# Kernel tuning notes

Measured on AMD Instinct MI355X. Metric: run time of the kernel, lower is better.

## Reference

```python
import jax, jax.numpy as jnp
import numpy as np

N_WAY = 5
K_SHOT = 5
TEMPERATURE = 0.2
EPS = 1e-12  # torch F.normalize eps


def setup_inputs() -> dict:
    key = jax.random.key(0)
    k1, k2, k3, k4 = jax.random.split(key, 4)
    b, q, c, h, w = 4, 75, 640, 10, 10
    s = N_WAY * K_SHOT
    return {
        "support_xf": jax.random.normal(k1, (b, s, c, h, w), dtype=jnp.float32),
        "support_y": jax.random.randint(k2, (b, s), 0, N_WAY),
        "query_xf": jax.random.normal(k3, (b, q, c, h, w), dtype=jnp.float32),
        "query_y": jax.random.randint(k4, (b, q), 0, N_WAY),
    }


def _l2norm(x):
    # normalize along last axis (channel), matching F.normalize semantics
    n = jnp.sqrt(jnp.sum(x * x, axis=-1, keepdims=True))
    return x / jnp.maximum(n, EPS)


def _inner_simi(support_xf, query_xf):
    # cosine similarity between all query local descriptors and all support
    # local descriptors, grouped per class -> [b, q, N, M_q, M_s]
    b, s, c, h, w = support_xf.shape
    q = query_xf.shape[1]
    hw = h * w
    Ms = K_SHOT * hw
    sx = support_xf.reshape(b, N_WAY, K_SHOT, c, hw)
    sx = jnp.transpose(sx, (0, 1, 2, 4, 3)).reshape(b, N_WAY, Ms, c)  # [b,N,M_s,c]
    qx = jnp.transpose(query_xf.reshape(b, q, c, hw), (0, 1, 3, 2))  # [b,q,M_q,c]
    return jnp.einsum('bqmc,bnsc->bqnms', _l2norm(qx), _l2norm(sx))


def _dmnn_mask(simi):
    # simi: [b,q,N,M_q,M_s] -> bool mask [b,q,M_q]
    b, q, N, Mq, Ms = simi.shape
    merged = jnp.transpose(simi, (0, 1, 3, 2, 4)).reshape(b, q, Mq, N * Ms)
    query_nearest = jnp.argmax(merged, axis=-1)            # [b,q,M_q] global NN idx
    class_max = jnp.max(simi, axis=-1)                      # [b,q,N,M_q]
    top2 = jax.lax.top_k(jnp.transpose(class_max, (0, 1, 3, 2)), 2)[0]  # [b,q,M_q,2]
    query_class_diff = top2[..., 0] - top2[..., 1]          # [b,q,M_q]
    diffs_m = jax.nn.one_hot(query_nearest, N * Ms, dtype=simi.dtype) \
        * query_class_diff[..., None]                       # [b,q,M_q,N*M_s]
    diffs_max_nearest = jnp.argmax(diffs_m, axis=-2)        # [b,q,N*M_s]
    gathered = jnp.take_along_axis(diffs_max_nearest, query_nearest, axis=-1)  # [b,q,M_q]
    return gathered == jnp.arange(Mq)[None, None, :]


def reference(support_xf, support_y, query_xf, query_y):
    b, q = query_xf.shape[0], query_xf.shape[1]
    simi = _inner_simi(support_xf, query_xf)                # [b,q,N,M_q,M_s]
    q_mask = _dmnn_mask(simi)                               # [b,q,M_q]
    class_max = jnp.max(simi, axis=-1)                      # [b,q,N,M_q]
    query_value = jnp.sum(class_max * q_mask[:, :, None, :].astype(simi.dtype), axis=-1)
    logits = query_value.reshape(b * q, N_WAY) / TEMPERATURE
    logp = jax.nn.log_softmax(logits, axis=-1)
    labels = query_y.reshape(b * q)
    loss = -jnp.mean(jnp.take_along_axis(logp, labels[:, None], axis=1))
    return loss
```

## Files before the change

kernel.cpp:

```cpp
#include <hip/hip_runtime.h>
#include <math.h>

#define B 4
#define Q 75
#define NBQ (B*Q)
#define NWAY 5
#define KSHOT 5
#define C 640
#define HW 100
#define MS 500
#define SLAB (C*HW)

#define MT32_B 236
#define RT_B 472
#define A_CHUNKS_B (RT_B*20*64)
#define S_CHUNKS_ALL (20*32*20*64)
#define S_CHUNKS_B   (5*32*20*64)

#define CHI 0.00390625f
#define CLO 1.9073486328125e-06f

typedef _Float16 half8 __attribute__((ext_vector_type(8)));
typedef float f32x4 __attribute__((ext_vector_type(4)));

__device__ __forceinline__ void gl_lds16(const void* gsrc, void* ldst) {
  __builtin_amdgcn_global_load_lds(
      (const __attribute__((address_space(1))) unsigned int*)gsrc,
      (__attribute__((address_space(3))) unsigned int*)ldst, 16, 0, 0);
}

#define WS_BASE 340352ull
#define NEED_ALL   104908288ull
#define NEED_PERB   46908928ull
#define NEED_PERB2  27248128ull

__global__ __launch_bounds__(256) void norm_kernel(const float* __restrict__ s_xf,
                                                   const float* __restrict__ q_xf,
                                                   float* __restrict__ invs,
                                                   float* __restrict__ invq) {
  int id = blockIdx.x;
  const float* base;
  float* out;
  if (id < 100) { base = s_xf + (size_t)id * SLAB;        out = invs + id * HW; }
  else          { base = q_xf + (size_t)(id - 100) * SLAB; out = invq + (id - 100) * HW; }
  __shared__ float ssum[2][HW];
  int t = threadIdx.x;
  if (t < 2 * HW) ((float*)ssum)[t] = 0.f;
  __syncthreads();
  if (t < 2 * HW) {
    int p = t % HW, half = t / HW;
    float part = 0.f;
    for (int ch = half * 320; ch < half * 320 + 320; ++ch) {
      float v = base[ch * HW + p];
      part = fmaf(v, v, part);
    }
    ssum[half][p] = part;
  }
  __syncthreads();
  if (t < HW) {
    float nrm = sqrtf(ssum[0][t] + ssum[1][t]);
    out[t] = 1.f / fmaxf(nrm, 1e-12f);
  }
}

__device__ __forceinline__ void dual_split(float w, _Float16* h0, _Float16* h1) {
  _Float16 a = (_Float16)w;
  *h0 = a;
  *h1 = (_Float16)((w - (float)a) * 2048.f);
}

__global__ __launch_bounds__(256) void convs_kernel(const float* __restrict__ s_xf,
                                                    const float* __restrict__ invs,
                                                    uint4* __restrict__ o0,
                                                    uint4* __restrict__ o1,
                                                    int bn0) {
  int id = blockIdx.x * 256 + threadIdx.x;
  int lane = id & 63;
  int tmp = id >> 6;
  int ks = tmp % 20;
  int t2 = tmp / 20;
  int jf = t2 % 32;
  int bnl = t2 / 32;
  int bn = bn0 + bnl;
  int j = jf * 16 + (lane & 15);
  int k = ks * 32 + (lane >> 4) * 8;
  union { _Float16 h[8]; uint4 u; } p0, p1;
  if (j < MS) {
    int s = j / 100, p = j % 100;
    int slab = bn * 5 + s;
    const float* src = s_xf + ((size_t)slab * 640 + k) * 100 + p;
    float sc = invs[slab * 100 + p] * 16.f;
#pragma unroll
    for (int kj = 0; kj < 8; ++kj)
      dual_split(src[kj * 100] * sc, &p0.h[kj], &p1.h[kj]);
  } else {
    p0.u = make_uint4(0, 0, 0, 0);
    p1.u = make_uint4(0, 0, 0, 0);
  }
  o0[id] = p0.u; o1[id] = p1.u;
}

__global__ __launch_bounds__(256) void convq_kernel(const float* __restrict__ q_xf,
                                                    const float* __restrict__ invq,
                                                    uint4* __restrict__ o0,
                                                    uint4* __restrict__ o1,
                                                    int b0) {
  int id = blockIdx.x * 256 + threadIdx.x;
  int bloc = id / A_CHUNKS_B;
  int c = id % A_CHUNKS_B;
  int bb = b0 + bloc;
  int lane = c & 63;
  int tmp = c >> 6;
  int ks = tmp % 20;
  int rt = tmp / 20;
  int row = rt * 16 + (lane & 15);
  int k = ks * 32 + (lane >> 4) * 8;
  union { _Float16 h[8]; uint4 u; } p0, p1;
  if (row < Q * HW) {
    int qi = row / 100, p = row % 100;
    const float* src = q_xf + ((size_t)(bb * Q + qi) * 640 + k) * 100 + p;
    float sc = invq[(bb * Q + qi) * 100 + p] * 16.f;
#pragma unroll
    for (int kj = 0; kj < 8; ++kj)
      dual_split(src[kj * 100] * sc, &p0.h[kj], &p1.h[kj]);
  } else {
    p0.u = make_uint4(0, 0, 0, 0);
    p1.u = make_uint4(0, 0, 0, 0);
  }
  o0[id] = p0.u; o1[id] = p1.u;
}

__global__ __launch_bounds__(256, 3) void gemm_kernel(
    const uint4* __restrict__ a0, const uint4* __restrict__ a1,
    const uint4* __restrict__ b0p, const uint4* __restrict__ b1p,
    float* __restrict__ cmax, int* __restrict__ carg,
    int bq0, int aStride, int sbnBase, int mode ) {
  int wgid = blockIdx.x;
  int x = wgid & 7, s = wgid >> 3;
  int o;
  if (mode == 0) {
    o = x * 590 + s;
  } else {
    if (x < 4) { if (s >= 148) return; o = x * 148 + s; }
    else       { if (s >= 147) return; o = 592 + (x - 4) * 147 + s; }
  }
  int bnloc = o / MT32_B;
  int mt32 = o % MT32_B;
  int bloc = bnloc / 5;
  int n = bnloc % 5;
  int bb = bq0 + bloc;
  const uint4* A0 = a0 + (size_t)bloc * aStride;
  const uint4* A1 = a1 + (size_t)bloc * aStride;
  int bnl = bb * 5 + n - sbnBase;

  __shared__ __align__(16) _Float16 sA[2][2][2][512];
  __shared__ float sV[4][32];
  __shared__ int   sJ[4][32];

  int t = threadIdx.x;
  int w = t >> 6, lane = t & 63;

  if (lane < 32) { sV[w][lane] = -1e30f; sJ[w][lane] = 0; }

#define STAGE_A1(KS, BUF) do {                                                  \
    int limb_ = w >> 1, rtl_ = w & 1;                                           \
    size_t aIdx = ((size_t)(mt32 * 2 + rtl_) * 20 + (KS)) * 64 + lane;          \
    gl_lds16((limb_ ? A1 : A0) + aIdx, (void*)&sA[(BUF)][limb_][rtl_][0]);      \
  } while (0)

  for (int pass = 0; pass < 2; ++pass) {
    int jf0 = pass * 16 + w * 4;
    size_t bBase = (size_t)(bnl * 32 + jf0) * 1280 + lane;

    f32x4 acc0[2][4], accM[2][4];
#pragma unroll
    for (int mf = 0; mf < 2; ++mf)
#pragma unroll
      for (int f = 0; f < 4; ++f) {
        acc0[mf][f] = (f32x4){0.f, 0.f, 0.f, 0.f};
        accM[mf][f] = (f32x4){0.f, 0.f, 0.f, 0.f};
      }

    STAGE_A1(0, 0);
    for (int ks = 0; ks < 20; ++ks) {
      int cur = ks & 1;
      __syncthreads();

      size_t bo = bBase + (size_t)ks * 64;
      half8 bv0[4], bv1[4];
#pragma unroll
      for (int f = 0; f < 4; ++f) bv0[f] = *(const half8*)&b0p[bo + (size_t)f * 1280];
#pragma unroll
      for (int f = 0; f < 4; ++f) bv1[f] = *(const half8*)&b1p[bo + (size_t)f * 1280];
      __builtin_amdgcn_sched_barrier(0);

      if (ks < 19) STAGE_A1(ks + 1, cur ^ 1);
      __builtin_amdgcn_sched_barrier(0);

#pragma unroll
      for (int mf = 0; mf < 2; ++mf) {
        half8 av0 = *(const half8*)&sA[cur][0][mf][lane * 8];
        half8 av1 = *(const half8*)&sA[cur][1][mf][lane * 8];
#pragma unroll
        for (int f = 0; f < 4; ++f) {
          acc0[mf][f] = __builtin_amdgcn_mfma_f32_16x16x32_f16(av0, bv0[f], acc0[mf][f], 0, 0, 0);
          accM[mf][f] = __builtin_amdgcn_mfma_f32_16x16x32_f16(av0, bv1[f], accM[mf][f], 0, 0, 0);
          accM[mf][f] = __builtin_amdgcn_mfma_f32_16x16x32_f16(av1, bv0[f], accM[mf][f], 0, 0, 0);
        }
      }
    }

#pragma unroll
    for (int mf = 0; mf < 2; ++mf)
#pragma unroll
      for (int f = 0; f < 4; ++f) {
        int j = pass * 256 + w * 64 + f * 16 + (lane & 15);
        bool ok = (j < MS);
#pragma unroll
        for (int rg = 0; rg < 4; ++rg) {
          float v = ok ? (acc0[mf][f][rg] * CHI + accM[mf][f][rg] * CLO) : -1e30f;
          int ji = ok ? j : 0x7fffffff;
#pragma unroll
          for (int mk = 1; mk < 16; mk <<= 1) {
            float ov = __shfl_xor(v, mk);
            int oj = __shfl_xor(ji, mk);
            if (ov > v || (ov == v && oj < ji)) { v = ov; ji = oj; }
          }
          if ((lane & 15) == 0) {
            int row32 = mf * 16 + (lane >> 4) * 4 + rg;
            if (v > sV[w][row32]) { sV[w][row32] = v; sJ[w][row32] = ji; }
          }
        }
      }
  }
#undef STAGE_A1

  __syncthreads();
  if (w == 0 && lane < 32) {
    int row32 = lane;
    float v = sV[0][row32];
    int ji = sJ[0][row32];
#pragma unroll
    for (int q4 = 1; q4 < 4; ++q4) {
      float ov = sV[q4][row32];
      int oj = sJ[q4][row32];
      if (ov > v || (ov == v && oj < ji)) { v = ov; ji = oj; }
    }
    int r = mt32 * 32 + row32;
    if (r < Q * HW) {
      int bq = bb * Q + r / 100, p = r % 100;
      size_t oo = (size_t)(bq * NWAY + n) * HW + p;
      cmax[oo] = v;
      carg[oo] = ji;
    }
  }
}

#define TCF 32
#define TJF 64
__global__ __launch_bounds__(256) void simi_kernel(const float* __restrict__ s_xf,
                                                   const float* __restrict__ q_xf,
                                                   const float* __restrict__ invs,
                                                   const float* __restrict__ invq,
                                                   float* __restrict__ cmax,
                                                   int* __restrict__ carg) {
  int id = blockIdx.x;
  int n = id % NWAY;
  int bq = id / NWAY;
  int b = bq / Q;
  const float* qbase = q_xf + (size_t)bq * SLAB;
  const float* sbase = s_xf + (size_t)(b * 25 + n * KSHOT) * SLAB;
  const float* invqB = invq + bq * HW;
  const float* invsB = invs + (b * 2500 + n * MS);

  __shared__ __align__(16) float As[TCF][112];
  __shared__ __align__(16) float Bs[TCF][TJF];
  __shared__ float sInvQ[HW];
  __shared__ float sInvS[MS];

  int t = threadIdx.x;
  for (int i = t; i < HW; i += 256) sInvQ[i] = invqB[i];
  for (int i = t; i < MS; i += 256) sInvS[i] = invsB[i];

  int tj = t & 15, tm = t >> 4;
  float best[7];
  int bidx[7];
#pragma unroll
  for (int r = 0; r < 7; ++r) { best[r] = -1e30f; bidx[r] = 0; }

  for (int jt0 = 0; jt0 < MS; jt0 += TJF) {
    float acc[7][4];
#pragma unroll
    for (int r = 0; r < 7; ++r)
#pragma unroll
      for (int jj = 0; jj < 4; ++jj) acc[r][jj] = 0.f;
    for (int c0 = 0; c0 < C; c0 += TCF) {
      __syncthreads();
      for (int i = t; i < TCF * HW; i += 256) {
        int p = i % HW;
        As[i / HW][p] = qbase[c0 * HW + i] * sInvQ[p];
      }
      for (int i = t; i < TCF * TJF; i += 256) {
        int cc = i / TJF, jj = i % TJF;
        int j = jt0 + jj;
        float v = 0.f;
        if (j < MS) v = sbase[(j / 100) * SLAB + (c0 + cc) * 100 + (j % 100)] * sInvS[j];
        Bs[cc][jj] = v;
      }
      __syncthreads();
#pragma unroll
      for (int cc = 0; cc < TCF; ++cc) {
        float4 bv = *(const float4*)&Bs[cc][tj * 4];
#pragma unroll
        for (int r = 0; r < 7; ++r) {
          float a = As[cc][tm * 7 + r];
          acc[r][0] = fmaf(a, bv.x, acc[r][0]);
          acc[r][1] = fmaf(a, bv.y, acc[r][1]);
          acc[r][2] = fmaf(a, bv.z, acc[r][2]);
          acc[r][3] = fmaf(a, bv.w, acc[r][3]);
        }
      }
    }
#pragma unroll
    for (int r = 0; r < 7; ++r)
#pragma unroll
      for (int jj = 0; jj < 4; ++jj) {
        int j = jt0 + tj * 4 + jj;
        float v = acc[r][jj];
        if (j < MS && v > best[r]) { best[r] = v; bidx[r] = j; }
      }
  }
#pragma unroll
  for (int r = 0; r < 7; ++r)
#pragma unroll
    for (int mask = 1; mask < 16; mask <<= 1) {
      float ov = __shfl_xor(best[r], mask);
      int oi = __shfl_xor(bidx[r], mask);
      if (ov > best[r] || (ov == best[r] && oi < bidx[r])) { best[r] = ov; bidx[r] = oi; }
    }
  if (tj == 0)
#pragma unroll
    for (int r = 0; r < 7; ++r) {
      int m = tm * 7 + r;
      if (m < HW) {
        cmax[(size_t)(bq * NWAY + n) * HW + m] = best[r];
        carg[(size_t)(bq * NWAY + n) * HW + m] = bidx[r];
      }
    }
}

__global__ __launch_bounds__(128) void mask_loss_kernel(const float* __restrict__ cmax,
                                                        const int* __restrict__ carg,
                                                        const int* __restrict__ query_y,
                                                        float* __restrict__ lossv) {
  int bq = blockIdx.x;
  int t = threadIdx.x;
  __shared__ float sDiff[HW];
  __shared__ int sNear[HW];
  __shared__ float sCm[NWAY][HW];
  __shared__ float red[128];

  if (t < HW) {
    float cm[NWAY];
#pragma unroll
    for (int nn = 0; nn < NWAY; ++nn) {
      cm[nn] = cmax[(size_t)(bq * NWAY + nn) * HW + t];
      sCm[nn][t] = cm[nn];
    }
    float v0 = -1e30f, v1 = -1e30f;
#pragma unroll
    for (int nn = 0; nn < NWAY; ++nn) {
      float v = cm[nn];
      if (v > v0) { v1 = v0; v0 = v; }
      else if (v > v1) { v1 = v; }
    }
    sDiff[t] = v0 - v1;
    float gb = -1e30f;
    int gn = 0;
#pragma unroll
    for (int nn = 0; nn < NWAY; ++nn)
      if (cm[nn] > gb) { gb = cm[nn]; gn = nn; }
    sNear[t] = gn * MS + carg[(size_t)(bq * NWAY + gn) * HW + t];
  }
  __syncthreads();

  bool msk = false;
  if (t < HW) {
    int j = sNear[t];
    int wn = 0;
    float wv = -1.f;
    for (int mp = 0; mp < HW; ++mp) {
      float v = (sNear[mp] == j) ? sDiff[mp] : 0.f;
      if (v > wv) { wv = v; wn = mp; }
    }
    msk = (wn == t);
  }

  float qv[NWAY];
#pragma unroll
  for (int nn = 0; nn < NWAY; ++nn) {
    __syncthreads();
    red[t] = (t < HW && msk) ? sCm[nn][t] : 0.f;
    __syncthreads();
    for (int s = 64; s > 0; s >>= 1) {
      if (t < s) red[t] += red[t + s];
      __syncthreads();
    }
    qv[nn] = red[0];
  }

  if (t == 0) {
    float logits[NWAY], mx = -1e30f;
#pragma unroll
    for (int nn = 0; nn < NWAY; ++nn) {
      logits[nn] = qv[nn] / 0.2f;
      mx = fmaxf(mx, logits[nn]);
    }
    float se = 0.f;
#pragma unroll
    for (int nn = 0; nn < NWAY; ++nn) se += expf(logits[nn] - mx);
    float lse = mx + logf(se);
    int label = query_y[bq];
    lossv[bq] = -(logits[label] - lse);
  }
}

__global__ __launch_bounds__(512) void finalize_kernel(const float* __restrict__ lossv,
                                                       float* __restrict__ out) {
  __shared__ float red[512];
  int t = threadIdx.x;
  red[t] = (t < NBQ) ? lossv[t] : 0.f;
  __syncthreads();
  for (int s = 256; s > 0; s >>= 1) {
    if (t < s) red[t] += red[t + s];
    __syncthreads();
  }
  if (t == 0) out[0] = red[0] / (float)NBQ;
}

extern "C" void kernel_launch(void* const* d_in, const int* in_sizes, int n_in,
                              void* d_out, int out_size, void* d_ws, size_t ws_size,
                              hipStream_t stream) {
  const float* s_xf = (const float*)d_in[0];
  const float* q_xf = (const float*)d_in[2];
  const int* query_y = (const int*)d_in[3];

  float* ws = (float*)d_ws;
  float* invs = ws;
  float* invq = ws + 10000;
  float* cmax = ws + 40000;
  int* carg = (int*)(ws + 190000);
  float* lossv = ws + 340000;

  norm_kernel<<<400, 256, 0, stream>>>(s_xf, q_xf, invs, invq);

  const size_t SP_ALL = 3276800, SP_B = 819200, QS_B = 2416640;

  if (ws_size >= NEED_ALL) {
    uint4* S0 = (uint4*)(ws + WS_BASE);
    uint4* S1 = (uint4*)(ws + WS_BASE + SP_ALL);
    uint4* Q0 = (uint4*)(ws + WS_BASE + 2 * SP_ALL);
    uint4* Q1 = (uint4*)(ws + WS_BASE + 2 * SP_ALL + 4 * QS_B);
    convs_kernel<<<S_CHUNKS_ALL / 256, 256, 0, stream>>>(s_xf, invs, S0, S1, 0);
    convq_kernel<<<4 * A_CHUNKS_B / 256, 256, 0, stream>>>(q_xf, invq, Q0, Q1, 0);
    gemm_kernel<<<4720, 256, 0, stream>>>(Q0, Q1, S0, S1,
                                          cmax, carg, 0, A_CHUNKS_B, 0, 0);
  } else if (ws_size >= NEED_PERB) {
    uint4* S0 = (uint4*)(ws + WS_BASE);
    uint4* S1 = (uint4*)(ws + WS_BASE + SP_ALL);
    uint4* Q0 = (uint4*)(ws + WS_BASE + 2 * SP_ALL);
    uint4* Q1 = (uint4*)(ws + WS_BASE + 2 * SP_ALL + QS_B);
    convs_kernel<<<S_CHUNKS_ALL / 256, 256, 0, stream>>>(s_xf, invs, S0, S1, 0);
    for (int b = 0; b < 4; ++b) {
      convq_kernel<<<A_CHUNKS_B / 256, 256, 0, stream>>>(q_xf, invq, Q0, Q1, b);
      gemm_kernel<<<1184, 256, 0, stream>>>(Q0, Q1, S0, S1,
                                            cmax, carg, b, 0, 0, 1);
    }
  } else if (ws_size >= NEED_PERB2) {
    uint4* S0 = (uint4*)(ws + WS_BASE);
    uint4* S1 = (uint4*)(ws + WS_BASE + SP_B);
    uint4* Q0 = (uint4*)(ws + WS_BASE + 2 * SP_B);
    uint4* Q1 = (uint4*)(ws + WS_BASE + 2 * SP_B + QS_B);
    for (int b = 0; b < 4; ++b) {
      convs_kernel<<<S_CHUNKS_B / 256, 256, 0, stream>>>(s_xf, invs, S0, S1, b * 5);
      convq_kernel<<<A_CHUNKS_B / 256, 256, 0, stream>>>(q_xf, invq, Q0, Q1, b);
      gemm_kernel<<<1184, 256, 0, stream>>>(Q0, Q1, S0, S1,
                                            cmax, carg, b, 0, b * 5, 1);
    }
  } else {
    simi_kernel<<<1500, 256, 0, stream>>>(s_xf, q_xf, invs, invq, cmax, carg);
  }

  mask_loss_kernel<<<NBQ, 128, 0, stream>>>(cmax, carg, query_y, lossv);
  finalize_kernel<<<1, 512, 0, stream>>>(lossv, (float*)d_out);
}
```

Measured before the change: 546.2 us.

## Load A fragments directly from global into registers instead of LDS staging

The GEMM kernel previously staged the A-operand tiles (hi/lo limbs) into a double-buffered LDS array via global_load_lds, with a block-wide barrier every k-step. Now each wave loads its own A fragments straight from global memory into registers and drops the barriers and the shared buffer. This removes the per-k-step synchronisation and the LDS traffic, but each of the four waves now fetches the same A data redundantly, relying on the cache. The loop is also kept rolled, so load latency is no longer explicitly overlapped.

```diff
diff --git a/kernel.cpp b/kernel.cpp
--- a/kernel.cpp
+++ b/kernel.cpp
@@ -22,12 +22,6 @@
 
 typedef _Float16 half8 __attribute__((ext_vector_type(8)));
 typedef float f32x4 __attribute__((ext_vector_type(4)));
-
-__device__ __forceinline__ void gl_lds16(const void* gsrc, void* ldst) {
-  __builtin_amdgcn_global_load_lds(
-      (const __attribute__((address_space(1))) unsigned int*)gsrc,
-      (__attribute__((address_space(3))) unsigned int*)ldst, 16, 0, 0);
-}
 
 #define WS_BASE 340352ull
 #define NEED_ALL   104908288ull
@@ -153,7 +147,6 @@
   const uint4* A1 = a1 + (size_t)bloc * aStride;
   int bnl = bb * 5 + n - sbnBase;
 
-  __shared__ __align__(16) _Float16 sA[2][2][2][512];
   __shared__ float sV[4][32];
   __shared__ int   sJ[4][32];
 
@@ -162,11 +155,7 @@
 
   if (lane < 32) { sV[w][lane] = -1e30f; sJ[w][lane] = 0; }
 
-#define STAGE_A1(KS, BUF) do {                                                  \
-    int limb_ = w >> 1, rtl_ = w & 1;                                           \
-    size_t aIdx = ((size_t)(mt32 * 2 + rtl_) * 20 + (KS)) * 64 + lane;          \
-    gl_lds16((limb_ ? A1 : A0) + aIdx, (void*)&sA[(BUF)][limb_][rtl_][0]);      \
-  } while (0)
+  size_t aBase = ((size_t)(mt32 * 2) * 20) * 64 + lane;
 
   for (int pass = 0; pass < 2; ++pass) {
     int jf0 = pass * 16 + w * 4;
@@ -181,10 +170,14 @@
         accM[mf][f] = (f32x4){0.f, 0.f, 0.f, 0.f};
       }
 
-    STAGE_A1(0, 0);
+#pragma unroll 1
     for (int ks = 0; ks < 20; ++ks) {
-      int cur = ks & 1;
-      __syncthreads();
+      size_t ao = aBase + (size_t)ks * 64;
+      half8 a0v[2], a1v[2];
+      a0v[0] = *(const half8*)&A0[ao];
+      a0v[1] = *(const half8*)&A0[ao + 1280];
+      a1v[0] = *(const half8*)&A1[ao];
+      a1v[1] = *(const half8*)&A1[ao + 1280];
 
       size_t bo = bBase + (size_t)ks * 64;
       half8 bv0[4], bv1[4];
@@ -192,20 +185,14 @@
       for (int f = 0; f < 4; ++f) bv0[f] = *(const half8*)&b0p[bo + (size_t)f * 1280];
 #pragma unroll
       for (int f = 0; f < 4; ++f) bv1[f] = *(const half8*)&b1p[bo + (size_t)f * 1280];
-      __builtin_amdgcn_sched_barrier(0);
-
-      if (ks < 19) STAGE_A1(ks + 1, cur ^ 1);
-      __builtin_amdgcn_sched_barrier(0);
 
 #pragma unroll
       for (int mf = 0; mf < 2; ++mf) {
-        half8 av0 = *(const half8*)&sA[cur][0][mf][lane * 8];
-        half8 av1 = *(const half8*)&sA[cur][1][mf][lane * 8];
 #pragma unroll
         for (int f = 0; f < 4; ++f) {
-          acc0[mf][f] = __builtin_amdgcn_mfma_f32_16x16x32_f16(av0, bv0[f], acc0[mf][f], 0, 0, 0);
-          accM[mf][f] = __builtin_amdgcn_mfma_f32_16x16x32_f16(av0, bv1[f], accM[mf][f], 0, 0, 0);
-          accM[mf][f] = __builtin_amdgcn_mfma_f32_16x16x32_f16(av1, bv0[f], accM[mf][f], 0, 0, 0);
+          acc0[mf][f] = __builtin_amdgcn_mfma_f32_16x16x32_f16(a0v[mf], bv0[f], acc0[mf][f], 0, 0, 0);
+          accM[mf][f] = __builtin_amdgcn_mfma_f32_16x16x32_f16(a0v[mf], bv1[f], accM[mf][f], 0, 0, 0);
+          accM[mf][f] = __builtin_amdgcn_mfma_f32_16x16x32_f16(a1v[mf], bv0[f], accM[mf][f], 0, 0, 0);
         }
       }
     }
@@ -233,7 +220,6 @@
         }
       }
   }
-#undef STAGE_A1
 
   __syncthreads();
   if (w == 0 && lane < 32) {
```

Result: slower. 673.5 us (+23.3%).
